# Kernel tuning notes

Measured on AMD Instinct MI355X. Metric: run time of the kernel, lower is better.

The kernel has to match this reference:

```python
import jax, jax.numpy as jnp
import numpy as np

H = 8          # num heads
D = 16         # head dim
HID = 128      # hidden_dim = H * D
NM, ND, NA = 100000, 20000, 50000
E = 300000     # edges per relation
NUM_CLASSES = 8


def setup_inputs() -> dict:
    key = jax.random.key(0)
    ks = jax.random.split(key, 24)
    s = 0.05
    eye = jnp.eye(D, dtype=jnp.float32)
    inp = {
        'x_movie': jax.random.normal(ks[0], (NM, 256), jnp.float32),
        'x_director': jax.random.normal(ks[1], (ND, 128), jnp.float32),
        'x_actor': jax.random.normal(ks[2], (NA, 128), jnp.float32),
        # edge lists per relation: (director->movie, actor->movie, movie->director, movie->actor)
        'src_dm': jax.random.randint(ks[3], (E,), 0, ND),
        'dst_dm': jax.random.randint(ks[4], (E,), 0, NM),
        'src_am': jax.random.randint(ks[5], (E,), 0, NA),
        'dst_am': jax.random.randint(ks[6], (E,), 0, NM),
        'src_md': jax.random.randint(ks[7], (E,), 0, NM),
        'dst_md': jax.random.randint(ks[8], (E,), 0, ND),
        'src_ma': jax.random.randint(ks[9], (E,), 0, NM),
        'dst_ma': jax.random.randint(ks[10], (E,), 0, NA),
        # per-type pre-encoder (use_pre_encoder=True)
        'Wpre_m': jax.random.normal(ks[11], (256, HID), jnp.float32) * s,
        'Wpre_d': jax.random.normal(ks[12], (128, HID), jnp.float32) * s,
        'Wpre_a': jax.random.normal(ks[13], (128, HID), jnp.float32) * s,
        'bpre': jnp.zeros((3, HID), jnp.float32),
        # per-type K/Q/V projections, stacked over the 3 node types
        'Wk': jax.random.normal(ks[14], (3, HID, HID), jnp.float32) * s,
        'bk': jnp.zeros((3, HID), jnp.float32),
        'Wq': jax.random.normal(ks[15], (3, HID, HID), jnp.float32) * s,
        'bq': jnp.zeros((3, HID), jnp.float32),
        'Wv': jax.random.normal(ks[16], (3, HID, HID), jnp.float32) * s,
        'bv': jnp.zeros((3, HID), jnp.float32),
        # per-relation attention / message matrices and priors (4 relations)
        'a_rel': eye + jax.random.normal(ks[17], (4, H, D, D), jnp.float32) * s,
        'm_rel': eye + jax.random.normal(ks[18], (4, H, D, D), jnp.float32) * s,
        'p_rel': jnp.ones((4, H), jnp.float32),
        # per-type skip gate and output projection
        'skip': jnp.ones((3,), jnp.float32),
        'Wa': jax.random.normal(ks[19], (3, HID, HID), jnp.float32) * s,
        'ba': jnp.zeros((3, HID), jnp.float32),
        # final classification head on target node type ('movie')
        'Wlin': jax.random.normal(ks[20], (HID, NUM_CLASSES), jnp.float32) * s,
        'blin': jnp.zeros((NUM_CLASSES,), jnp.float32),
    }
    return inp


def _seg_softmax_agg(alpha, msg, dst, n):
    # softmax over incoming edges of each destination node, then weighted sum of msgs
    m = jax.ops.segment_max(alpha, dst, num_segments=n)      # [n, H]
    m = jnp.where(jnp.isfinite(m), m, 0.0)
    a = jnp.exp(alpha - m[dst])                              # [E, H]
    denom = jax.ops.segment_sum(a, dst, num_segments=n)      # [n, H]
    num = jax.ops.segment_sum(a[:, :, None] * msg, dst, num_segments=n)  # [n, H, D]
    return num / jnp.maximum(denom, 1e-16)[:, :, None]


def reference(x_movie, x_director, x_actor,
              src_dm, dst_dm, src_am, dst_am, src_md, dst_md, src_ma, dst_ma,
              Wpre_m, Wpre_d, Wpre_a, bpre, Wk, bk, Wq, bq, Wv, bv,
              a_rel, m_rel, p_rel, skip, Wa, ba, Wlin, blin):
    # type order: 0=movie, 1=director, 2=actor
    xs = [x_movie @ Wpre_m + bpre[0],
          x_director @ Wpre_d + bpre[1],
          x_actor @ Wpre_a + bpre[2]]
    k = [(x @ Wk[t] + bk[t]).reshape(-1, H, D) for t, x in enumerate(xs)]
    q = [(x @ Wq[t] + bq[t]).reshape(-1, H, D) for t, x in enumerate(xs)]
    v = [(x @ Wv[t] + bv[t]).reshape(-1, H, D) for t, x in enumerate(xs)]

    # (src_type, dst_type, src_idx, dst_idx) per relation
    rels = [(1, 0, src_dm, dst_dm), (2, 0, src_am, dst_am),
            (0, 1, src_md, dst_md), (0, 2, src_ma, dst_ma)]
    scale = 1.0 / np.sqrt(D).astype(np.float32)
    buckets = {0: [], 1: [], 2: []}
    for r, (st, dt, src, dst) in enumerate(rels):
        ke = jnp.einsum('ehd,hdf->ehf', k[st][src], a_rel[r])          # [E,H,D]
        al = jnp.einsum('ehf,ehf->eh', q[dt][dst], ke) * p_rel[r] * scale
        me = jnp.einsum('ehd,hdf->ehf', v[st][src], m_rel[r])          # [E,H,D]
        buckets[dt].append((al, me, dst))

    n = [x.shape[0] for x in xs]
    outs = []
    for t in range(3):
        al = jnp.concatenate([b[0] for b in buckets[t]], axis=0)
        me = jnp.concatenate([b[1] for b in buckets[t]], axis=0)
        dst = jnp.concatenate([b[2] for b in buckets[t]], axis=0)
        agg = _seg_softmax_agg(al, me, dst, n[t]).reshape(n[t], HID)
        h = jax.nn.gelu(agg, approximate=False) @ Wa[t] + ba[t]
        g = jax.nn.sigmoid(skip[t])
        outs.append(g * h + (1.0 - g) * xs[t])

    return outs[0] @ Wlin + blin
```

## Files before the change

kernel.cpp:

```cpp
#include <hip/hip_runtime.h>
#include <hip/hip_bf16.h>
#include <math.h>

#define NM 100000
#define ND 20000
#define NA 50000
#define EDG 300000
#define CAP 32

#define NTM 6250
#define NTD 1250
#define NTA 3125
#define MB  391
#define DB  79
#define AB  196

typedef __attribute__((ext_vector_type(8))) short shortx8;
typedef __attribute__((ext_vector_type(4))) float floatx4;
typedef __attribute__((ext_vector_type(4))) int intx4;

__device__ __forceinline__ float bf2f(unsigned int u) {
    return __uint_as_float(u << 16);
}
__device__ __forceinline__ unsigned short f2bf(float f) {
    unsigned int x = __float_as_uint(f);
    unsigned int r = x + 0x7fffu + ((x >> 16) & 1u);
    return (unsigned short)(r >> 16);
}
__device__ __forceinline__ unsigned short f2bf_fast(float f) {
    return (unsigned short)((__float_as_uint(f) + 0x8000u) >> 16);
}
__device__ __forceinline__ unsigned int pkbf2(float a, float b) {
    return __builtin_amdgcn_perm(__float_as_uint(b) + 0x8000u,
                                 __float_as_uint(a) + 0x8000u,
                                 0x07060302u);
}
__device__ __forceinline__ shortx8 pack8(floatx4 a, floatx4 b) {
    intx4 r;
    r[0] = (int)pkbf2(a[0], a[1]);
    r[1] = (int)pkbf2(a[2], a[3]);
    r[2] = (int)pkbf2(b[0], b[1]);
    r[3] = (int)pkbf2(b[2], b[3]);
    return __builtin_bit_cast(shortx8, r);
}
__device__ __forceinline__ float gelu_exact(float x) {
    return 0.5f * x * (1.0f + erff(x * 0.70710678118654752f));
}

static const size_t OFF_BT_Q      = 0;
static const size_t OFF_BT_KAMV_D = 73728;
static const size_t OFF_BT_KAMV_A = 139264;
static const size_t OFF_WKA_D     = 204800;
static const size_t OFF_WVM_D     = 270336;
static const size_t OFF_WKA_A     = 335872;
static const size_t OFF_WVM_A     = 401408;
static const size_t OFF_BQ        = 466944;
static const size_t OFF_B_KAMV_D  = 467520;
static const size_t OFF_B_KAMV_A  = 468544;
static const size_t OFF_BKA_D     = 469568;
static const size_t OFF_BVM_D     = 470080;
static const size_t OFF_BKA_A     = 470592;
static const size_t OFF_BVM_A     = 471104;
static const size_t OFF_WALS      = 471616;
static const size_t OFF_BFIN      = 475712;
static const size_t OFF_Q0        = 524288;
static const size_t OFF_SKIPB     = 26124288;
static const size_t OFF_WQT       = 26124288;
static const size_t OFF_KAMV_D    = 29324288;
static const size_t OFF_KAMV_A    = 39564288;
static const size_t OFF_COUNTS    = 65164288;
static const size_t OFF_SLOTS     = 65564288;
#define KAMV_A_DELTA 10240000

__global__ __launch_bounds__(256) void precompA(
    const float* __restrict__ Wk, const float* __restrict__ bk,
    const float* __restrict__ Wv, const float* __restrict__ bv,
    const float* __restrict__ Wa, const float* __restrict__ ba,
    const float* __restrict__ Wlin, const float* __restrict__ blin,
    const float* __restrict__ a_rel, const float* __restrict__ m_rel,
    const float* __restrict__ p_rel, const float* __restrict__ skip,
    const float* __restrict__ bpre, const float* __restrict__ Wq,
    char* __restrict__ ws)
{
    int tid = blockIdx.x * 256 + threadIdx.x;
    if (tid < 65536) {
        int mat = tid >> 14, rem = tid & 16383;
        int e = rem >> 7, hf = rem & 127, h = hf >> 4, f = hf & 15;
        const float* Wsrc; const float* R; float sc; float* dst;
        if (mat == 0)      { Wsrc = Wk + 16384; R = a_rel;        sc = p_rel[h]     * 0.25f; dst = (float*)(ws + OFF_WKA_D); }
        else if (mat == 1) { Wsrc = Wv + 16384; R = m_rel;        sc = 1.0f;                 dst = (float*)(ws + OFF_WVM_D); }
        else if (mat == 2) { Wsrc = Wk + 32768; R = a_rel + 2048; sc = p_rel[8 + h] * 0.25f; dst = (float*)(ws + OFF_WKA_A); }
        else               { Wsrc = Wv + 32768; R = m_rel + 2048; sc = 1.0f;                 dst = (float*)(ws + OFF_WVM_A); }
        float s = 0.0f;
        for (int d = 0; d < 16; d++)
            s += Wsrc[e * 128 + h * 16 + d] * R[h * 256 + d * 16 + f];
        dst[hf * 128 + e] = s * sc;
    } else if (tid < 66048) {
        int idx = tid - 65536;
        int mat = idx >> 7, hf = idx & 127, h = hf >> 4, f = hf & 15;
        const float* bsrc; const float* R; float sc; float* dst;
        if (mat == 0)      { bsrc = bk + 128; R = a_rel;        sc = p_rel[h]     * 0.25f; dst = (float*)(ws + OFF_BKA_D); }
        else if (mat == 1) { bsrc = bv + 128; R = m_rel;        sc = 1.0f;                 dst = (float*)(ws + OFF_BVM_D); }
        else if (mat == 2) { bsrc = bk + 256; R = a_rel + 2048; sc = p_rel[8 + h] * 0.25f; dst = (float*)(ws + OFF_BKA_A); }
        else               { bsrc = bv + 256; R = m_rel + 2048; sc = 1.0f;                 dst = (float*)(ws + OFF_BVM_A); }
        float s = 0.0f;
        for (int d = 0; d < 16; d++)
            s += bsrc[h * 16 + d] * R[h * 256 + d * 16 + f];
        dst[hf] = s * sc;
    } else if (tid < 67072) {
        int idx = tid - 66048;
        int j = idx >> 3, c = idx & 7;
        float g = 1.0f / (1.0f + __expf(-skip[0]));
        float s = 0.0f;
        for (int o = 0; o < 128; o++)
            s += Wa[j * 128 + o] * Wlin[o * 8 + c];
        ((float*)(ws + OFF_WALS))[j * 8 + c] = g * s;
    } else if (tid < 67080) {
        int c = tid - 67072;
        float g = 1.0f / (1.0f + __expf(-skip[0]));
        float s1 = 0.0f, s2 = 0.0f;
        for (int o = 0; o < 128; o++) {
            s1 += ba[o]   * Wlin[o * 8 + c];
            s2 += bpre[o] * Wlin[o * 8 + c];
        }
        ((float*)(ws + OFF_BFIN))[c] = g * s1 + (1.0f - g) * s2 + blin[c];
    } else if (tid < 83464) {
        int i = tid - 67080;
        int n = i >> 7, e = i & 127;
        ((float*)(ws + OFF_WQT))[n * 128 + e] = Wq[e * 128 + n];
    } else if (tid < 83464 + NM) {
        ((int*)(ws + OFF_COUNTS))[tid - 83464] = 0;
    }
}

__device__ __forceinline__ float dot128(const float* __restrict__ a,
                                        const float* __restrict__ b) {
    const floatx4* x = (const floatx4*)a;
    const floatx4* y = (const floatx4*)b;
    float s = 0.0f;
    #pragma unroll
    for (int i = 0; i < 32; i++) {
        floatx4 u = x[i], v = y[i];
        s += u[0] * v[0] + u[1] * v[1] + u[2] * v[2] + u[3] * v[3];
    }
    return s;
}

__global__ __launch_bounds__(256) void prep_scat(
    const int* __restrict__ src_dm, const int* __restrict__ dst_dm,
    const int* __restrict__ src_am, const int* __restrict__ dst_am,
    const float* __restrict__ Wpre_m, const float* __restrict__ Wpre_d,
    const float* __restrict__ Wpre_a, const float* __restrict__ bpre,
    const float* __restrict__ bq, const float* __restrict__ Wlin,
    const float* __restrict__ skip,
    char* __restrict__ ws)
{
    if (blockIdx.x < 2344) {
        int t = blockIdx.x * 256 + threadIdx.x;
        if (t >= 2 * EDG) return;
        int src, dst, delta;
        if (t < EDG) { src = src_dm[t];       dst = dst_dm[t];       delta = 0; }
        else         { src = src_am[t - EDG]; dst = dst_am[t - EDG]; delta = KAMV_A_DELTA; }
        int* counts = (int*)(ws + OFF_COUNTS);
        int* slots  = (int*)(ws + OFF_SLOTS);
        int pos = atomicAdd(&counts[dst], 1);
        if (pos < CAP) slots[(size_t)dst * CAP + pos] = src * 512 + delta;
        return;
    }
    int tid = (blockIdx.x - 2344) * 256 + threadIdx.x;
    const float* WKA_D = (const float*)(ws + OFF_WKA_D);
    const float* WVM_D = (const float*)(ws + OFF_WVM_D);
    const float* WKA_A = (const float*)(ws + OFF_WKA_A);
    const float* WVM_A = (const float*)(ws + OFF_WVM_A);
    const float* WqT   = (const float*)(ws + OFF_WQT);

    if (tid < 36864) {
        int n = tid >> 8, c = tid & 255;
        float s = 0.0f;
        if (n < 128) {
            s = dot128(Wpre_m + c * 128, WqT + n * 128);
        } else if (n < 136) {
            int cc = n - 128;
            float g = 1.0f / (1.0f + __expf(-skip[0]));
            for (int e = 0; e < 128; e++)
                s += Wpre_m[c * 128 + e] * Wlin[e * 8 + cc];
            s *= (1.0f - g);
        }
        ((unsigned short*)(ws + OFF_BT_Q))[(c >> 7) * 18432 + n * 128 + (c & 127)] = f2bf(s);
    } else if (tid < 69632) {
        int idx = tid - 36864;
        int nrow = idx >> 7, c = idx & 127;
        const float* WfT = (nrow < 128) ? WKA_D : WVM_D;
        int nc = nrow & 127;
        float s = dot128(Wpre_d + c * 128, WfT + nc * 128);
        ((unsigned short*)(ws + OFF_BT_KAMV_D))[nrow * 128 + c] = f2bf(s);
    } else if (tid < 102400) {
        int idx = tid - 69632;
        int nrow = idx >> 7, c = idx & 127;
        const float* WfT = (nrow < 128) ? WKA_A : WVM_A;
        int nc = nrow & 127;
        float s = dot128(Wpre_a + c * 128, WfT + nc * 128);
        ((unsigned short*)(ws + OFF_BT_KAMV_A))[nrow * 128 + c] = f2bf(s);
    } else if (tid < 102544) {
        int n = tid - 102400;
        float s = 0.0f;
        if (n < 128) s = dot128(bpre, WqT + n * 128) + bq[n];
        ((float*)(ws + OFF_BQ))[n] = s;
    } else if (tid < 102800) {
        int nrow = tid - 102544;
        const float* WfT = (nrow < 128) ? WKA_D : WVM_D;
        const float* bf_ = (nrow < 128) ? (const float*)(ws + OFF_BKA_D) : (const float*)(ws + OFF_BVM_D);
        int nc = nrow & 127;
        ((float*)(ws + OFF_B_KAMV_D))[nrow] = dot128(bpre + 128, WfT + nc * 128) + bf_[nc];
    } else if (tid < 103056) {
        int nrow = tid - 102800;
        const float* WfT = (nrow < 128) ? WKA_A : WVM_A;
        const float* bf_ = (nrow < 128) ? (const float*)(ws + OFF_BKA_A) : (const float*)(ws + OFF_BVM_A);
        int nc = nrow & 127;
        ((float*)(ws + OFF_B_KAMV_A))[nrow] = dot128(bpre + 256, WfT + nc * 128) + bf_[nc];
    }
}

#define MFMA16(a, b, c) __builtin_amdgcn_mfma_f32_16x16x32_bf16(a, b, c, 0, 0, 0)

__global__ __launch_bounds__(256, 2) void gemm_all(
    const float* __restrict__ xm, const float* __restrict__ xd,
    const float* __restrict__ xa,
    const unsigned short* __restrict__ btq,
    const unsigned short* __restrict__ btd,
    const unsigned short* __restrict__ bta,
    const float* __restrict__ bq,
    const float* __restrict__ bbd, const float* __restrict__ bba,
    unsigned short* __restrict__ q0, float* __restrict__ skipb,
    unsigned short* __restrict__ outd, unsigned short* __restrict__ outa)
{
    __shared__ unsigned short b_lds[288 * 136];
    int tid = threadIdx.x;
    int w = tid >> 6, lane = tid & 63;
    int quad = lane >> 4, low = lane & 15;
    int bx = blockIdx.x;

    if (bx < MB) {
        #pragma unroll
        for (int it = 0; it < 18; it++) {
            int idx = it * 256 + tid, r = idx >> 4, ch = idx & 15;
            *(intx4*)&b_lds[r * 136 + ch * 8] =
                *(const intx4*)&btq[(size_t)r * 128 + ch * 8];
        }
        __syncthreads();
        float bqr[9];
        #pragma unroll
        for (int j = 0; j < 9; j++) bqr[j] = bq[j * 16 + low];

        int t0 = (bx * 4 + w) * 4;
        floatx4 st[16];
        {
            int te = t0 < NTM ? t0 : NTM - 1;
            const float* Ap = xm + (size_t)(te * 16 + low) * 256 + quad * 8;
            #pragma unroll
            for (int ks = 0; ks < 8; ks++) {
                st[2 * ks]     = *(const floatx4*)(Ap + ks * 32);
                st[2 * ks + 1] = *(const floatx4*)(Ap + ks * 32 + 4);
            }
        }
        #pragma unroll
        for (int i = 0; i < 4; i++) {
            int t = t0 + i;
            shortx8 fa[8];
            #pragma unroll
            for (int ks = 0; ks < 8; ks++) fa[ks] = pack8(st[2 * ks], st[2 * ks + 1]);
            {
                int tn = t + 1 < NTM ? t + 1 : NTM - 1;
                const float* Ap = xm + (size_t)(tn * 16 + low) * 256 + quad * 8;
                #pragma unroll
                for (int ks = 0; ks < 8; ks++) {
                    st[2 * ks]     = *(const floatx4*)(Ap + ks * 32);
                    st[2 * ks + 1] = *(const floatx4*)(Ap + ks * 32 + 4);
                }
            }
            floatx4 acc[9] = {};
            #pragma unroll
            for (int ks = 0; ks < 8; ks++) {
                int rb = (ks >> 2) * 19584 + low * 136 + (ks & 3) * 32 + quad * 8;
                #pragma unroll
                for (int j = 0; j < 9; j++) {
                    shortx8 b = *(const shortx8*)&b_lds[rb + j * 2176];
                    acc[j] = MFMA16(fa[ks], b, acc[j]);
                }
            }
            if (t < NTM) {
                int row0 = t * 16 + quad * 4;
                #pragma unroll
                for (int j = 0; j < 8; j++) {
                    int col = j * 16 + low;
                    #pragma unroll
                    for (int r = 0; r < 4; r++)
                        q0[(size_t)(row0 + r) * 128 + col] = f2bf_fast(acc[j][r] + bqr[j]);
                }
                if (low < 8) {
                    #pragma unroll
                    for (int r = 0; r < 4; r++)
                        skipb[(size_t)(row0 + r) * 8 + low] = acc[8][r] + bqr[8];
                }
            }
        }
    } else {
        const float* A; const unsigned short* BT; const float* bias;
        unsigned short* outb; int ntt, wid;
        if (bx < MB + DB) { A = xd; BT = btd; bias = bbd; outb = outd; ntt = NTD; wid = (bx - MB) * 4 + w; }
        else              { A = xa; BT = bta; bias = bba; outb = outa; ntt = NTA; wid = (bx - MB - DB) * 4 + w; }
        #pragma unroll
        for (int it = 0; it < 16; it++) {
            int idx = it * 256 + tid, r = idx >> 4, ch = idx & 15;
            *(intx4*)&b_lds[r * 136 + ch * 8] =
                *(const intx4*)&BT[(size_t)r * 128 + ch * 8];
        }
        __syncthreads();
        float biasr[16];
        #pragma unroll
        for (int j = 0; j < 16; j++) biasr[j] = bias[j * 16 + low];

        int t0 = wid * 4;
        floatx4 st[8];
        {
            int te = t0 < ntt ? t0 : ntt - 1;
            const float* Ap = A + (size_t)(te * 16 + low) * 128 + quad * 8;
            #pragma unroll
            for (int ks = 0; ks < 4; ks++) {
                st[2 * ks]     = *(const floatx4*)(Ap + ks * 32);
                st[2 * ks + 1] = *(const floatx4*)(Ap + ks * 32 + 4);
            }
        }
        #pragma unroll
        for (int i = 0; i < 4; i++) {
            int t = t0 + i;
            shortx8 fa[4];
            #pragma unroll
            for (int ks = 0; ks < 4; ks++) fa[ks] = pack8(st[2 * ks], st[2 * ks + 1]);
            {
                int tn = t + 1 < ntt ? t + 1 : ntt - 1;
                const float* Ap = A + (size_t)(tn * 16 + low) * 128 + quad * 8;
                #pragma unroll
                for (int ks = 0; ks < 4; ks++) {
                    st[2 * ks]     = *(const floatx4*)(Ap + ks * 32);
                    st[2 * ks + 1] = *(const floatx4*)(Ap + ks * 32 + 4);
                }
            }
            floatx4 acc[16] = {};
            #pragma unroll
            for (int ks = 0; ks < 4; ks++) {
                int rb = low * 136 + ks * 32 + quad * 8;
                #pragma unroll
                for (int j = 0; j < 16; j++) {
                    shortx8 b = *(const shortx8*)&b_lds[rb + j * 2176];
                    acc[j] = MFMA16(fa[ks], b, acc[j]);
                }
            }
            if (t < ntt) {
                int row0 = t * 16 + quad * 4;
                #pragma unroll
                for (int j = 0; j < 16; j++) {
                    int col = j * 16 + low;
                    #pragma unroll
                    for (int r = 0; r < 4; r++)
                        outb[(size_t)(row0 + r) * 256 + col] = f2bf_fast(acc[j][r] + biasr[j]);
                }
            }
        }
    }
}

__global__ __launch_bounds__(256) void agg_kernel(
    const unsigned short* __restrict__ q0,
    const char* __restrict__ kamv0,
    const int* __restrict__ counts, const int* __restrict__ slots,
    const float* __restrict__ skipb,
    const float* __restrict__ WaLs, const float* __restrict__ bfin,
    float* __restrict__ out)
{
    __shared__ float wals[1032];
    for (int i = threadIdx.x; i < 1024; i += 256) {
        int c = i >> 7, rem = i & 127, j = rem >> 4, L = rem & 15;
        wals[i] = WaLs[(L * 8 + j) * 8 + c];
    }
    if (threadIdx.x < 8) wals[1024 + threadIdx.x] = bfin[threadIdx.x];
    __syncthreads();

    int lane = threadIdx.x & 63;
    int grp = lane >> 4;
    int L   = lane & 15;
    int n = blockIdx.x * 16 + (threadIdx.x >> 6) * 4 + grp;

    intx4 qv = *(const intx4*)(q0 + (size_t)n * 128 + L * 8);
    float qf[8];
    #pragma unroll
    for (int d = 0; d < 4; d++) {
        unsigned int u = (unsigned int)qv[d];
        qf[2 * d]     = __uint_as_float(u << 16);
        qf[2 * d + 1] = __uint_as_float(u & 0xffff0000u);
    }

    int cnt = counts[n];
    cnt = cnt < 0 ? 0 : (cnt > CAP ? CAP : cnt);
    int s0 = slots[(size_t)n * CAP + L];

    float acc[8] = {0, 0, 0, 0, 0, 0, 0, 0};
    float den = 0.0f;
    if (cnt > 0) {
        int off0 = __shfl(s0, lane & 48);
        const char* p = kamv0 + off0;
        intx4 ku = *(const intx4*)(p + L * 16);
        intx4 mu = *(const intx4*)(p + 256 + L * 16);
        for (int i = 0; i < cnt; i++) {
            int inext = (i + 1 < cnt) ? i + 1 : i;
            int offn = __shfl(s0, (lane & 48) + (inext & 15));
            if (__builtin_expect(inext >= 16, 0)) offn = slots[(size_t)n * CAP + inext];
            const char* pn = kamv0 + offn;
            intx4 kun = *(const intx4*)(pn + L * 16);
            intx4 mun = *(const intx4*)(pn + 256 + L * 16);

            float ph = 0.0f;
            #pragma unroll
            for (int d = 0; d < 4; d++) {
                unsigned int u = (unsigned int)ku[d];
                ph += qf[2 * d]     * __uint_as_float(u << 16);
                ph += qf[2 * d + 1] * __uint_as_float(u & 0xffff0000u);
            }
            float pf = ph + __shfl_xor(ph, 1);
            float wgt = __expf(fminf(pf, 60.0f));
            den += wgt;
            #pragma unroll
            for (int d = 0; d < 4; d++) {
                unsigned int u = (unsigned int)mu[d];
                acc[2 * d]     += wgt * __uint_as_float(u << 16);
                acc[2 * d + 1] += wgt * __uint_as_float(u & 0xffff0000u);
            }
            ku = kun; mu = mun;
        }
    }
    float inv = 1.0f / fmaxf(den, 1e-16f);

    float part[8] = {0, 0, 0, 0, 0, 0, 0, 0};
    #pragma unroll
    for (int j = 0; j < 8; j++) {
        float u = gelu_exact(acc[j] * inv);
        #pragma unroll
        for (int c = 0; c < 8; c++)
            part[c] += u * wals[c * 128 + j * 16 + L];
    }

    bool b0 = lane & 1, b1 = lane & 2, b2 = lane & 4;
    float t1[4], t2[2], t3;
    #pragma unroll
    for (int k = 0; k < 4; k++) {
        float send = b0 ? part[k] : part[4 + k];
        float got  = __shfl_xor(send, 1);
        t1[k] = (b0 ? part[4 + k] : part[k]) + got;
    }
    #pragma unroll
    for (int k = 0; k < 2; k++) {
        float send = b1 ? t1[k] : t1[2 + k];
        float got  = __shfl_xor(send, 2);
        t2[k] = (b1 ? t1[2 + k] : t1[k]) + got;
    }
    {
        float send = b2 ? t2[0] : t2[1];
        float got  = __shfl_xor(send, 4);
        t3 = (b2 ? t2[1] : t2[0]) + got;
    }
    t3 += __shfl_xor(t3, 8);
    if (L < 8) {
        int c = 4 * (L & 1) + 2 * ((L >> 1) & 1) + ((L >> 2) & 1);
        out[(size_t)n * 8 + c] = t3 + skipb[(size_t)n * 8 + c] + wals[1024 + c];
    }
}

extern "C" void kernel_launch(void* const* d_in, const int* in_sizes, int n_in,
                              void* d_out, int out_size, void* d_ws, size_t ws_size,
                              hipStream_t stream) {
    (void)in_sizes; (void)n_in; (void)out_size; (void)ws_size;
    const float* x_movie    = (const float*)d_in[0];
    const float* x_director = (const float*)d_in[1];
    const float* x_actor    = (const float*)d_in[2];
    const int* src_dm = (const int*)d_in[3];
    const int* dst_dm = (const int*)d_in[4];
    const int* src_am = (const int*)d_in[5];
    const int* dst_am = (const int*)d_in[6];
    const float* Wpre_m = (const float*)d_in[11];
    const float* Wpre_d = (const float*)d_in[12];
    const float* Wpre_a = (const float*)d_in[13];
    const float* bpre   = (const float*)d_in[14];
    const float* Wk     = (const float*)d_in[15];
    const float* bk     = (const float*)d_in[16];
    const float* Wq     = (const float*)d_in[17];
    const float* bq     = (const float*)d_in[18];
    const float* Wv     = (const float*)d_in[19];
    const float* bv     = (const float*)d_in[20];
    const float* a_rel  = (const float*)d_in[21];
    const float* m_rel  = (const float*)d_in[22];
    const float* p_rel  = (const float*)d_in[23];
    const float* skip   = (const float*)d_in[24];
    const float* Wa     = (const float*)d_in[25];
    const float* ba     = (const float*)d_in[26];
    const float* Wlin   = (const float*)d_in[27];
    const float* blin   = (const float*)d_in[28];

    char* ws = (char*)d_ws;
    float* out = (float*)d_out;

    precompA<<<(83464 + NM + 255) / 256, 256, 0, stream>>>(
        Wk, bk, Wv, bv, Wa, ba, Wlin, blin,
        a_rel, m_rel, p_rel, skip, bpre, Wq, ws);

    prep_scat<<<2344 + 403, 256, 0, stream>>>(
        src_dm, dst_dm, src_am, dst_am,
        Wpre_m, Wpre_d, Wpre_a, bpre, bq, Wlin, skip, ws);

    gemm_all<<<MB + DB + AB, 256, 0, stream>>>(
        x_movie, x_director, x_actor,
        (const unsigned short*)(ws + OFF_BT_Q),
        (const unsigned short*)(ws + OFF_BT_KAMV_D),
        (const unsigned short*)(ws + OFF_BT_KAMV_A),
        (const float*)(ws + OFF_BQ),
        (const float*)(ws + OFF_B_KAMV_D), (const float*)(ws + OFF_B_KAMV_A),
        (unsigned short*)(ws + OFF_Q0), (float*)(ws + OFF_SKIPB),
        (unsigned short*)(ws + OFF_KAMV_D), (unsigned short*)(ws + OFF_KAMV_A));

    agg_kernel<<<NM / 16, 256, 0, stream>>>(
        (const unsigned short*)(ws + OFF_Q0),
        (const char*)(ws + OFF_KAMV_D),
        (const int*)(ws + OFF_COUNTS), (const int*)(ws + OFF_SLOTS),
        (const float*)(ws + OFF_SKIPB),
        (const float*)(ws + OFF_WALS), (const float*)(ws + OFF_BFIN), out);
}
```

Before: 377.3 us.

## Deepen A-tile prefetch, widen per-wave tiles, and restride LDS in gemm_all

Each wave now handles 6 row tiles instead of 4 and keeps two register staging buffers, so global loads run two tiles ahead of the MFMA work. The grid shrinks to match. The LDS B layout changes to a single 272-element row stride for the movie path and a 144 stride for the director/actor paths, which changes bank-conflict behaviour. Outputs are written with nontemporal stores. Costs are higher register pressure from the doubled staging arrays, which could hurt occupancy under launch_bounds(256,2), and fewer blocks to spread over the CUs.

```diff
diff --git a/kernel.cpp b/kernel.cpp
--- a/kernel.cpp
+++ b/kernel.cpp
@@ -11,9 +11,10 @@
 #define NTM 6250
 #define NTD 1250
 #define NTA 3125
-#define MB  391
-#define DB  79
-#define AB  196
+#define T_W 6
+#define MB3 261
+#define DB3 53
+#define AB3 131
 
 typedef __attribute__((ext_vector_type(8))) short shortx8;
 typedef __attribute__((ext_vector_type(4))) float floatx4;
@@ -223,6 +224,28 @@
 
 #define MFMA16(a, b, c) __builtin_amdgcn_mfma_f32_16x16x32_bf16(a, b, c, 0, 0, 0)
 
+__device__ __forceinline__ void stage_m(floatx4 (&buf)[16], const float* __restrict__ xm,
+                                        int te, int low, int quad) {
+    te = te < NTM ? te : NTM - 1;
+    const float* Ap = xm + (size_t)(te * 16 + low) * 256 + quad * 8;
+    #pragma unroll
+    for (int ks = 0; ks < 8; ks++) {
+        buf[2 * ks]     = *(const floatx4*)(Ap + ks * 32);
+        buf[2 * ks + 1] = *(const floatx4*)(Ap + ks * 32 + 4);
+    }
+}
+
+__device__ __forceinline__ void stage_k(floatx4 (&buf)[8], const float* __restrict__ A,
+                                        int te, int ntt, int low, int quad) {
+    te = te < ntt ? te : ntt - 1;
+    const float* Ap = A + (size_t)(te * 16 + low) * 128 + quad * 8;
+    #pragma unroll
+    for (int ks = 0; ks < 4; ks++) {
+        buf[2 * ks]     = *(const floatx4*)(Ap + ks * 32);
+        buf[2 * ks + 1] = *(const floatx4*)(Ap + ks * 32 + 4);
+    }
+}
+
 __global__ __launch_bounds__(256, 2) void gemm_all(
     const float* __restrict__ xm, const float* __restrict__ xd,
     const float* __restrict__ xa,
@@ -234,57 +257,45 @@
     unsigned short* __restrict__ q0, float* __restrict__ skipb,
     unsigned short* __restrict__ outd, unsigned short* __restrict__ outa)
 {
-    __shared__ unsigned short b_lds[288 * 136];
+    __shared__ unsigned short b_lds[144 * 272];
     int tid = threadIdx.x;
     int w = tid >> 6, lane = tid & 63;
     int quad = lane >> 4, low = lane & 15;
     int bx = blockIdx.x;
 
-    if (bx < MB) {
+    if (bx < MB3) {
         #pragma unroll
         for (int it = 0; it < 18; it++) {
-            int idx = it * 256 + tid, r = idx >> 4, ch = idx & 15;
-            *(intx4*)&b_lds[r * 136 + ch * 8] =
-                *(const intx4*)&btq[(size_t)r * 128 + ch * 8];
+            int h = it / 9;
+            int rem = (it % 9) * 256 + tid;
+            int n = rem >> 4, ch = rem & 15;
+            *(intx4*)&b_lds[n * 272 + h * 128 + ch * 8] =
+                *(const intx4*)&btq[(size_t)h * 18432 + n * 128 + ch * 8];
         }
         __syncthreads();
         float bqr[9];
         #pragma unroll
         for (int j = 0; j < 9; j++) bqr[j] = bq[j * 16 + low];
 
-        int t0 = (bx * 4 + w) * 4;
-        floatx4 st[16];
-        {
-            int te = t0 < NTM ? t0 : NTM - 1;
-            const float* Ap = xm + (size_t)(te * 16 + low) * 256 + quad * 8;
-            #pragma unroll
-            for (int ks = 0; ks < 8; ks++) {
-                st[2 * ks]     = *(const floatx4*)(Ap + ks * 32);
-                st[2 * ks + 1] = *(const floatx4*)(Ap + ks * 32 + 4);
-            }
-        }
-        #pragma unroll
-        for (int i = 0; i < 4; i++) {
+        int t0 = (bx * 4 + w) * T_W;
+        floatx4 st[2][16];
+        stage_m(st[0], xm, t0,     low, quad);
+        stage_m(st[1], xm, t0 + 1, low, quad);
+        #pragma unroll
+        for (int i = 0; i < T_W; i++) {
             int t = t0 + i;
             shortx8 fa[8];
             #pragma unroll
-            for (int ks = 0; ks < 8; ks++) fa[ks] = pack8(st[2 * ks], st[2 * ks + 1]);
-            {
-                int tn = t + 1 < NTM ? t + 1 : NTM - 1;
-                const float* Ap = xm + (size_t)(tn * 16 + low) * 256 + quad * 8;
-                #pragma unroll
-                for (int ks = 0; ks < 8; ks++) {
-                    st[2 * ks]     = *(const floatx4*)(Ap + ks * 32);
-                    st[2 * ks + 1] = *(const floatx4*)(Ap + ks * 32 + 4);
-                }
-            }
+            for (int ks = 0; ks < 8; ks++)
+                fa[ks] = pack8(st[i & 1][2 * ks], st[i & 1][2 * ks + 1]);
+            stage_m(st[i & 1], xm, t0 + i + 2, low, quad);
             floatx4 acc[9] = {};
             #pragma unroll
             for (int ks = 0; ks < 8; ks++) {
-                int rb = (ks >> 2) * 19584 + low * 136 + (ks & 3) * 32 + quad * 8;
+                int kb = ks * 32 + quad * 8;
                 #pragma unroll
                 for (int j = 0; j < 9; j++) {
-                    shortx8 b = *(const shortx8*)&b_lds[rb + j * 2176];
+                    shortx8 b = *(const shortx8*)&b_lds[(j * 16 + low) * 272 + kb];
                     acc[j] = MFMA16(fa[ks], b, acc[j]);
                 }
             }
@@ -295,24 +306,27 @@
                     int col = j * 16 + low;
                     #pragma unroll
                     for (int r = 0; r < 4; r++)
-                        q0[(size_t)(row0 + r) * 128 + col] = f2bf_fast(acc[j][r] + bqr[j]);
+                        __builtin_nontemporal_store(f2bf_fast(acc[j][r] + bqr[j]),
+                            &q0[(size_t)(row0 + r) * 128 + col]);
                 }
                 if (low < 8) {
                     #pragma unroll
                     for (int r = 0; r < 4; r++)
-                        skipb[(size_t)(row0 + r) * 8 + low] = acc[8][r] + bqr[8];
+                        __builtin_nontemporal_store(acc[8][r] + bqr[8],
+                            &skipb[(size_t)(row0 + r) * 8 + low]);
                 }
             }
         }
     } else {
         const float* A; const unsigned short* BT; const float* bias;
         unsigned short* outb; int ntt, wid;
-        if (bx < MB + DB) { A = xd; BT = btd; bias = bbd; outb = outd; ntt = NTD; wid = (bx - MB) * 4 + w; }
-        else              { A = xa; BT = bta; bias = bba; outb = outa; ntt = NTA; wid = (bx - MB - DB) * 4 + w; }
+        if (bx < MB3 + DB3) { A = xd; BT = btd; bias = bbd; outb = outd; ntt = NTD; wid = (bx - MB3) * 4 + w; }
+        else                { A = xa; BT = bta; bias = bba; outb = outa; ntt = NTA; wid = (bx - MB3 - DB3) * 4 + w; }
         #pragma unroll
         for (int it = 0; it < 16; it++) {
-            int idx = it * 256 + tid, r = idx >> 4, ch = idx & 15;
-            *(intx4*)&b_lds[r * 136 + ch * 8] =
+            int idx = it * 256 + tid;
+            int r = idx >> 4, ch = idx & 15;
+            *(intx4*)&b_lds[r * 144 + ch * 8] =
                 *(const intx4*)&BT[(size_t)r * 128 + ch * 8];
         }
         __syncthreads();
@@ -320,39 +334,25 @@
         #pragma unroll
         for (int j = 0; j < 16; j++) biasr[j] = bias[j * 16 + low];
 
-        int t0 = wid * 4;
-        floatx4 st[8];
-        {
-            int te = t0 < ntt ? t0 : ntt - 1;
-            const float* Ap = A + (size_t)(te * 16 + low) * 128 + quad * 8;
-            #pragma unroll
-            for (int ks = 0; ks < 4; ks++) {
-                st[2 * ks]     = *(const floatx4*)(Ap + ks * 32);
-                st[2 * ks + 1] = *(const floatx4*)(Ap + ks * 32 + 4);
-            }
-        }
-        #pragma unroll
-        for (int i = 0; i < 4; i++) {
+        int t0 = wid * T_W;
+        floatx4 st[2][8];
+        stage_k(st[0], A, t0,     ntt, low, quad);
+        stage_k(st[1], A, t0 + 1, ntt, low, quad);
+        #pragma unroll
+        for (int i = 0; i < T_W; i++) {
             int t = t0 + i;
             shortx8 fa[4];
             #pragma unroll
-            for (int ks = 0; ks < 4; ks++) fa[ks] = pack8(st[2 * ks], st[2 * ks + 1]);
-            {
-                int tn = t + 1 < ntt ? t + 1 : ntt - 1;
-                const float* Ap = A + (size_t)(tn * 16 + low) * 128 + quad * 8;
-                #pragma unroll
-                for (int ks = 0; ks < 4; ks++) {
-                    st[2 * ks]     = *(const floatx4*)(Ap + ks * 32);
-                    st[2 * ks + 1] = *(const floatx4*)(Ap + ks * 32 + 4);
-                }
-            }
+            for (int ks = 0; ks < 4; ks++)
+                fa[ks] = pack8(st[i & 1][2 * ks], st[i & 1][2 * ks + 1]);
+            stage_k(st[i & 1], A, t0 + i + 2, ntt, low, quad);
             floatx4 acc[16] = {};
             #pragma unroll
             for (int ks = 0; ks < 4; ks++) {
-                int rb = low * 136 + ks * 32 + quad * 8;
+                int kb = ks * 32 + quad * 8;
                 #pragma unroll
                 for (int j = 0; j < 16; j++) {
-                    shortx8 b = *(const shortx8*)&b_lds[rb + j * 2176];
+                    shortx8 b = *(const shortx8*)&b_lds[(j * 16 + low) * 144 + kb];
                     acc[j] = MFMA16(fa[ks], b, acc[j]);
                 }
             }
@@ -516,7 +516,7 @@
         src_dm, dst_dm, src_am, dst_am,
         Wpre_m, Wpre_d, Wpre_a, bpre, bq, Wlin, skip, ws);
 
-    gemm_all<<<MB + DB + AB, 256, 0, stream>>>(
+    gemm_all<<<MB3 + DB3 + AB3, 256, 0, stream>>>(
         x_movie, x_director, x_actor,
         (const unsigned short*)(ws + OFF_BT_Q),
         (const unsigned short*)(ws + OFF_BT_KAMV_D),
```

After: 396.1 us. 5.0% more time.
